# Kernel optimization log

Measured on AMD Instinct MI355X. Metric: run time of the kernel, lower is better.

Reference implementation:

```python
import jax, jax.numpy as jnp
import numpy as np

B, N, C = 1024, 65, 1024
H = 16
D = C // H  # head dim = 64
HIDDEN = 4 * C
EPS = 1e-5


def layer_norm(x, g, b):
    mu = jnp.mean(x, axis=-1, keepdims=True)
    var = jnp.var(x, axis=-1, keepdims=True)
    return (x - mu) * jax.lax.rsqrt(var + EPS) * g + b


def setup_inputs() -> dict:
    key = jax.random.key(0)
    ks = jax.random.split(key, 12)
    s = 0.02
    return {
        "x": jax.random.normal(ks[0], (B, N, C), dtype=jnp.float32),
        "ln1_g": jnp.ones((C,), jnp.float32),
        "ln1_b": jnp.zeros((C,), jnp.float32),
        "qkv_w": jax.random.normal(ks[1], (3 * C, C), jnp.float32) * s,
        "qkv_b": jnp.zeros((3 * C,), jnp.float32),
        "proj_w": jax.random.normal(ks[2], (C, C), jnp.float32) * s,
        "proj_b": jnp.zeros((C,), jnp.float32),
        "attn_bias": jax.random.normal(ks[3], (H, N, N), jnp.float32) * 0.1,
        "bias_scale": jnp.asarray(1.0, jnp.float32),
        "ln2_g": jnp.ones((C,), jnp.float32),
        "ln2_b": jnp.zeros((C,), jnp.float32),
        "fc1_w": jax.random.normal(ks[4], (HIDDEN, C), jnp.float32) * s,
        "fc1_b": jnp.zeros((HIDDEN,), jnp.float32),
        "fc2_w": jax.random.normal(ks[5], (C, HIDDEN), jnp.float32) * s,
        "fc2_b": jnp.zeros((C,), jnp.float32),
    }


def reference(x, ln1_g, ln1_b, qkv_w, qkv_b, proj_w, proj_b, attn_bias,
              bias_scale, ln2_g, ln2_b, fc1_w, fc1_b, fc2_w, fc2_b):
    scale = D ** -0.5
    # --- attention branch: pre-LN ---
    h = layer_norm(x, ln1_g, ln1_b)
    qkv = h @ qkv_w.T + qkv_b                      # [B,N,3C]
    qkv = qkv.reshape(B, N, 3, H, D)
    q = jnp.transpose(qkv[:, :, 0], (0, 2, 1, 3))  # [B,H,N,D]
    k = jnp.transpose(qkv[:, :, 1], (0, 2, 1, 3))
    v = jnp.transpose(qkv[:, :, 2], (0, 2, 1, 3))
    logits = jnp.einsum('bhnd,bhmd->bhnm', q, k) * scale
    logits = logits + bias_scale * attn_bias[None]  # learned per-head 65x65 bias
    attn = jax.nn.softmax(logits, axis=-1)
    o = jnp.einsum('bhnm,bhmd->bhnd', attn, v)      # [B,H,N,D]
    o = jnp.transpose(o, (0, 2, 1, 3)).reshape(B, N, C)
    x = x + (o @ proj_w.T + proj_b)
    # --- MLP branch: pre-LN ---
    h = layer_norm(x, ln2_g, ln2_b)
    h = h @ fc1_w.T + fc1_b
    h = jax.nn.gelu(h, approximate=True)            # tanh GELU, matches F.gelu(approximate='tanh')
    h = h @ fc2_w.T + fc2_b
    return x + h
```

## Files before the change

kernel.cpp:

```cpp
#include <hip/hip_runtime.h>
#include <hip/hip_bf16.h>
#include <cstdint>

typedef __attribute__((ext_vector_type(8))) short bf16x8;
typedef __attribute__((ext_vector_type(8))) unsigned short ushort8;
typedef __attribute__((ext_vector_type(4))) float f32x4;

__device__ __forceinline__ unsigned short f2bf(float f) {
    unsigned u = __builtin_bit_cast(unsigned, f);
    u += 0x7FFFu + ((u >> 16) & 1u);
    return (unsigned short)(u >> 16);
}
__device__ __forceinline__ float bf2f(unsigned short s) {
    unsigned u = ((unsigned)s) << 16;
    return __builtin_bit_cast(float, u);
}

__device__ __forceinline__ void gld16(const unsigned short* g, unsigned short* l) {
    __builtin_amdgcn_global_load_lds(
        (const __attribute__((address_space(1))) void*)g,
        (__attribute__((address_space(3))) void*)l, 16, 0, 0);
}

#define BARRIER    asm volatile("s_barrier" ::: "memory")
#define WAITLGKM0  asm volatile("s_waitcnt lgkmcnt(0)" ::: "memory")
#define WAITVM6    asm volatile("s_waitcnt vmcnt(6)" ::: "memory")

__global__ __launch_bounds__(256) void cvt_w(const float* __restrict__ s,
                                             unsigned short* __restrict__ d, int n4) {
    int i = blockIdx.x * 256 + threadIdx.x;
    if (i >= n4) return;
    float4 v = ((const float4*)s)[i];
    ushort4 o = make_ushort4(f2bf(v.x), f2bf(v.y), f2bf(v.z), f2bf(v.w));
    ((ushort4*)d)[i] = o;
}

__global__ __launch_bounds__(256) void ln_bf16(const float* __restrict__ x,
                                               const float* __restrict__ g,
                                               const float* __restrict__ bta,
                                               unsigned short* __restrict__ out) {
    const int row = blockIdx.x;
    const int t = threadIdx.x;
    const float4 v = ((const float4*)(x + (size_t)row * 1024))[t];
    float s  = v.x + v.y + v.z + v.w;
    float ss = v.x*v.x + v.y*v.y + v.z*v.z + v.w*v.w;
#pragma unroll
    for (int off = 32; off > 0; off >>= 1) {
        s  += __shfl_down(s,  off, 64);
        ss += __shfl_down(ss, off, 64);
    }
    __shared__ float red[8];
    if ((t & 63) == 0) { red[t >> 6] = s; red[4 + (t >> 6)] = ss; }
    __syncthreads();
    const float S  = red[0] + red[1] + red[2] + red[3];
    const float SS = red[4] + red[5] + red[6] + red[7];
    const float mu = S * (1.0f / 1024.0f);
    const float rs = rsqrtf(SS * (1.0f / 1024.0f) - mu * mu + 1e-5f);
    const float4 gv = ((const float4*)g)[t];
    const float4 bv = ((const float4*)bta)[t];
    ushort4 o = make_ushort4(f2bf((v.x - mu) * rs * gv.x + bv.x),
                             f2bf((v.y - mu) * rs * gv.y + bv.y),
                             f2bf((v.z - mu) * rs * gv.z + bv.z),
                             f2bf((v.w - mu) * rs * gv.w + bv.w));
    ((ushort4*)(out + (size_t)row * 1024))[t] = o;
}

template <int MODE>
__global__ __launch_bounds__(512, 2) void gemm8p(const unsigned short* __restrict__ A,
                                                 const unsigned short* __restrict__ W,
                                                 const float* __restrict__ bias,
                                                 const float* __restrict__ res,
                                                 void* __restrict__ outv,
                                                 int N, int K) {
    __shared__ __align__(128) unsigned short lA[4][8192];
    __shared__ __align__(128) unsigned short lB[4][8192];
    const int t = threadIdx.x;
    const int lane = t & 63;
    const int wave = t >> 6;
    const int wm = wave >> 2, wn = wave & 3;

    const int nwg  = gridDim.x * gridDim.y;
    const int orig = blockIdx.y * gridDim.x + blockIdx.x;
    const int id   = (orig & 7) * (nwg >> 3) + (orig >> 3);
    const int bx   = id % gridDim.x;
    const int by   = id / gridDim.x;
    const long row0 = (long)by * 256;
    const long col0 = (long)bx * 256;

    const int srow  = wave * 16 + (lane >> 3);
    const int sslot = (lane & 7) ^ ((lane >> 3) & 7);
    const unsigned short* gA = A + (row0 + srow) * (long)K + sslot * 8;
    const unsigned short* gW = W + (col0 + srow) * (long)K + sslot * 8;
    const int lwo = wave * 1024;

#define STG_A(H, TILE, SLOT) do { \
    const unsigned short* _g = gA + (long)(H) * 128 * K + (long)(TILE) * 64; \
    unsigned short* _l = &lA[(SLOT) * 2 + (H)][lwo]; \
    gld16(_g, _l); gld16(_g + 8L * K, _l + 512); } while (0)
#define STG_B(H, TILE, SLOT) do { \
    const unsigned short* _g = gW + (long)(H) * 128 * K + (long)(TILE) * 64; \
    unsigned short* _l = &lB[(SLOT) * 2 + (H)][lwo]; \
    gld16(_g, _l); gld16(_g + 8L * K, _l + 512); } while (0)

    const int NT = K >> 6;
    const int I  = NT >> 1;

    const int arow = lane & 15;
    const int khi  = lane >> 4;
    const int low7 = lane & 7;

    f32x4 acc[8][4] = {};
    bf16x8 af[4][2], bf0[2][2], bf1[2][2];

    STG_A(0, 0, 0); STG_B(0, 0, 0); STG_B(1, 0, 0); STG_A(1, 0, 0);
    STG_A(0, 1, 1); STG_B(0, 1, 1); STG_B(1, 1, 1);
    WAITVM6;
    BARRIER;

    for (int j = 0; j < I; ++j) {
        const bool stN = (j + 1) < I;
#pragma unroll
        for (int tp = 0; tp < 2; ++tp) {
            const int s2 = tp * 2;
            const int tN = 2 * j + 2 + tp;
            const bool stA1 = (2 * j + tp + 1) < NT;

#pragma unroll
            for (int fi = 0; fi < 4; ++fi) {
                const int r = wm * 64 + fi * 16 + arow;
#pragma unroll
                for (int ks = 0; ks < 2; ++ks)
                    af[fi][ks] = *(const bf16x8*)&lA[s2][r * 64 + (((ks * 4 + khi) ^ low7) << 3)];
            }
#pragma unroll
            for (int fj = 0; fj < 2; ++fj) {
                const int r = wn * 32 + fj * 16 + arow;
#pragma unroll
                for (int ks = 0; ks < 2; ++ks)
                    bf0[fj][ks] = *(const bf16x8*)&lB[s2][r * 64 + (((ks * 4 + khi) ^ low7) << 3)];
            }
            if (stA1) STG_A(1, 2 * j + tp + 1, tp ^ 1);
            BARRIER;
            __builtin_amdgcn_s_setprio(1);
#pragma unroll
            for (int fi = 0; fi < 4; ++fi)
#pragma unroll
                for (int fj = 0; fj < 2; ++fj)
#pragma unroll
                    for (int ks = 0; ks < 2; ++ks)
                        acc[fi][fj] = __builtin_amdgcn_mfma_f32_16x16x32_bf16(af[fi][ks], bf0[fj][ks], acc[fi][fj], 0, 0, 0);
            __builtin_amdgcn_s_setprio(0);
            WAITLGKM0;
            BARRIER;

#pragma unroll
            for (int fj = 0; fj < 2; ++fj) {
                const int r = wn * 32 + fj * 16 + arow;
#pragma unroll
                for (int ks = 0; ks < 2; ++ks)
                    bf1[fj][ks] = *(const bf16x8*)&lB[s2 + 1][r * 64 + (((ks * 4 + khi) ^ low7) << 3)];
            }
            if (stN) STG_A(0, tN, tp);
            BARRIER;
            __builtin_amdgcn_s_setprio(1);
#pragma unroll
            for (int fi = 0; fi < 4; ++fi)
#pragma unroll
                for (int fj = 0; fj < 2; ++fj)
#pragma unroll
                    for (int ks = 0; ks < 2; ++ks)
                        acc[fi][2 + fj] = __builtin_amdgcn_mfma_f32_16x16x32_bf16(af[fi][ks], bf1[fj][ks], acc[fi][2 + fj], 0, 0, 0);
            __builtin_amdgcn_s_setprio(0);
            WAITLGKM0;
            BARRIER;

#pragma unroll
            for (int fi = 0; fi < 4; ++fi) {
                const int r = wm * 64 + fi * 16 + arow;
#pragma unroll
                for (int ks = 0; ks < 2; ++ks)
                    af[fi][ks] = *(const bf16x8*)&lA[s2 + 1][r * 64 + (((ks * 4 + khi) ^ low7) << 3)];
            }
            if (stN) STG_B(0, tN, tp);
            BARRIER;
            __builtin_amdgcn_s_setprio(1);
#pragma unroll
            for (int fi = 0; fi < 4; ++fi)
#pragma unroll
                for (int fj = 0; fj < 2; ++fj)
#pragma unroll
                    for (int ks = 0; ks < 2; ++ks)
                        acc[4 + fi][2 + fj] = __builtin_amdgcn_mfma_f32_16x16x32_bf16(af[fi][ks], bf1[fj][ks], acc[4 + fi][2 + fj], 0, 0, 0);
            __builtin_amdgcn_s_setprio(0);
            WAITLGKM0;
            BARRIER;

            if (stN) STG_B(1, tN, tp);
            BARRIER;
            __builtin_amdgcn_s_setprio(1);
#pragma unroll
            for (int fi = 0; fi < 4; ++fi)
#pragma unroll
                for (int fj = 0; fj < 2; ++fj)
#pragma unroll
                    for (int ks = 0; ks < 2; ++ks)
                        acc[4 + fi][fj] = __builtin_amdgcn_mfma_f32_16x16x32_bf16(af[fi][ks], bf0[fj][ks], acc[4 + fi][fj], 0, 0, 0);
            __builtin_amdgcn_s_setprio(0);
            WAITVM6;
            WAITLGKM0;
            BARRIER;
        }
    }

    const int r4 = khi * 4;
#pragma unroll
    for (int jj = 0; jj < 4; ++jj) {
        const long col = col0 + (jj >> 1) * 128 + wn * 32 + (jj & 1) * 16 + arow;
        const float bj = bias[col];
#pragma unroll
        for (int i = 0; i < 8; ++i) {
            const long rowb = row0 + (i >> 2) * 128 + wm * 64 + (i & 3) * 16 + r4;
#pragma unroll
            for (int r = 0; r < 4; ++r) {
                const long row = rowb + r;
                float val = acc[i][jj][r] + bj;
                if (MODE == 2) {
                    float u = 1.5957691216057308f * (val + 0.044715f * val * val * val);
                    float e = __expf(u);
                    float th = 1.0f - 2.0f / (e + 1.0f);
                    val = 0.5f * val * (1.0f + th);
                }
                if (MODE == 1) {
                    ((float*)outv)[row * N + col] = res[row * N + col] + val;
                } else {
                    ((unsigned short*)outv)[row * N + col] = f2bf(val);
                }
            }
        }
    }
#undef STG_A
#undef STG_B
}

#define SSTR 68
__global__ __launch_bounds__(256) void attn(const unsigned short* __restrict__ qkv,
                                            const float* __restrict__ abias,
                                            const float* __restrict__ bscale_p,
                                            unsigned short* __restrict__ o) {
    const int bh = blockIdx.x;
    const int b = bh >> 4, h = bh & 15;
    const int t = threadIdx.x;
    __shared__ __align__(16) float sq[65 * SSTR];
    __shared__ __align__(16) float sk[65 * SSTR];
    __shared__ __align__(16) unsigned short sv[65 * SSTR];
    __shared__ float ss[65 * 65];
    const size_t base = (size_t)b * 65 * 3072 + h * 64;
    for (int idx = t; idx < 65 * 64; idx += 256) {
        int n = idx >> 6, d = idx & 63;
        size_t g = base + (size_t)n * 3072 + d;
        sq[n * SSTR + d] = bf2f(qkv[g]);
        sk[n * SSTR + d] = bf2f(qkv[g + 1024]);
        sv[n * SSTR + d] = qkv[g + 2048];
    }
    __syncthreads();
    const float bs = bscale_p[0];
    const float* bias_h = abias + h * 65 * 65;
    for (int p = t; p < 65 * 65; p += 256) {
        int i = p % 65, j = p / 65;
        const float4* q4 = (const float4*)&sq[i * SSTR];
        const float4* k4 = (const float4*)&sk[j * SSTR];
        float ax = 0.f, ay = 0.f, az = 0.f, aw = 0.f;
#pragma unroll
        for (int c = 0; c < 16; c++) {
            float4 a = q4[c], bb = k4[c];
            ax += a.x * bb.x; ay += a.y * bb.y; az += a.z * bb.z; aw += a.w * bb.w;
        }
        ss[i * 65 + j] = (ax + ay + az + aw) * 0.125f + bs * bias_h[i * 65 + j];
    }
    __syncthreads();
    if (t < 65) {
        float* r = &ss[t * 65];
        float m = -1e30f;
        for (int j = 0; j < 65; j++) m = fmaxf(m, r[j]);
        float sum = 0.f;
        for (int j = 0; j < 65; j++) { float e = __expf(r[j] - m); r[j] = e; sum += e; }
        float inv = 1.0f / sum;
        for (int j = 0; j < 65; j++) r[j] *= inv;
    }
    __syncthreads();
    for (int p = t; p < 65 * 16; p += 256) {
        int i = p % 65, d4 = p / 65;
        float ax = 0.f, ay = 0.f, az = 0.f, aw = 0.f;
        for (int j = 0; j < 65; j++) {
            float pv = ss[i * 65 + j];
            ushort4 vv = *(const ushort4*)&sv[j * SSTR + d4 * 4];
            ax += pv * bf2f(vv.x); ay += pv * bf2f(vv.y);
            az += pv * bf2f(vv.z); aw += pv * bf2f(vv.w);
        }
        size_t go = (size_t)(b * 65 + i) * 1024 + h * 64 + d4 * 4;
        *(ushort4*)&o[go] = make_ushort4(f2bf(ax), f2bf(ay), f2bf(az), f2bf(aw));
    }
}

extern "C" void kernel_launch(void* const* d_in, const int* in_sizes, int n_in,
                              void* d_out, int out_size, void* d_ws, size_t ws_size,
                              hipStream_t stream) {
    const float* x      = (const float*)d_in[0];
    const float* ln1_g  = (const float*)d_in[1];
    const float* ln1_b  = (const float*)d_in[2];
    const float* qkv_w  = (const float*)d_in[3];
    const float* qkv_b  = (const float*)d_in[4];
    const float* proj_w = (const float*)d_in[5];
    const float* proj_b = (const float*)d_in[6];
    const float* abias  = (const float*)d_in[7];
    const float* bscale = (const float*)d_in[8];
    const float* ln2_g  = (const float*)d_in[9];
    const float* ln2_b  = (const float*)d_in[10];
    const float* fc1_w  = (const float*)d_in[11];
    const float* fc1_b  = (const float*)d_in[12];
    const float* fc2_w  = (const float*)d_in[13];
    const float* fc2_b  = (const float*)d_in[14];
    float* out = (float*)d_out;

    char* ws = (char*)d_ws;
    unsigned short* qkvbuf = (unsigned short*)(ws);
    unsigned short* hbuf   = (unsigned short*)(ws + 545259520ULL);
    unsigned short* wqkv   = (unsigned short*)(ws + 681574400ULL);
    unsigned short* wproj  = (unsigned short*)(ws + 687865856ULL);
    unsigned short* wfc1   = (unsigned short*)(ws + 689963008ULL);
    unsigned short* wfc2   = (unsigned short*)(ws + 698351616ULL);

    const int M = 66560;

    cvt_w<<<3072, 256, 0, stream>>>(qkv_w,  wqkv,  786432);
    cvt_w<<<1024, 256, 0, stream>>>(proj_w, wproj, 262144);
    cvt_w<<<4096, 256, 0, stream>>>(fc1_w,  wfc1,  1048576);
    cvt_w<<<4096, 256, 0, stream>>>(fc2_w,  wfc2,  1048576);

    ln_bf16<<<M, 256, 0, stream>>>(x, ln1_g, ln1_b, hbuf);
    gemm8p<0><<<dim3(12, 260), 512, 0, stream>>>(hbuf, wqkv, qkv_b, nullptr,
                                                 (void*)qkvbuf, 3072, 1024);
    attn<<<16384, 256, 0, stream>>>(qkvbuf, abias, bscale, hbuf);
    gemm8p<1><<<dim3(4, 260), 512, 0, stream>>>(hbuf, wproj, proj_b, x,
                                                (void*)out, 1024, 1024);
    ln_bf16<<<M, 256, 0, stream>>>(out, ln2_g, ln2_b, hbuf);
    gemm8p<2><<<dim3(16, 260), 512, 0, stream>>>(hbuf, wfc1, fc1_b, nullptr,
                                                 (void*)qkvbuf, 4096, 1024);
    gemm8p<1><<<dim3(4, 260), 512, 0, stream>>>(qkvbuf, wfc2, fc2_b, out,
                                                (void*)out, 1024, 4096);
}
```

Before: 3.720 ms.

## Rewrite attention kernel with MFMA tiles for QK^T and PV

Replaces the scalar fp32 attention kernel with one that computes QK^T and P·V using 16x16x32 bf16 MFMA instructions on 16-row tiles padded to 80 rows and 96 columns. Q and K are staged in LDS as bf16 with 16-byte loads, and V is stored transposed with zero padding. Softmax is spread over four lanes per row with shuffle reductions, writes unnormalised bf16 probabilities, and applies the 1/sum scale at output. The change is meant to cut the per-head dot-product cost and LDS traffic. In exchange, probabilities are rounded to bf16 before P·V, and the kernel uses more LDS with aliased buffers.

```diff
diff --git a/kernel.cpp b/kernel.cpp
--- a/kernel.cpp
+++ b/kernel.cpp
@@ -242,63 +242,117 @@
 #undef STG_B
 }
 
-#define SSTR 68
-__global__ __launch_bounds__(256) void attn(const unsigned short* __restrict__ qkv,
-                                            const float* __restrict__ abias,
-                                            const float* __restrict__ bscale_p,
-                                            unsigned short* __restrict__ o) {
+__global__ __launch_bounds__(256, 3) void attn_mfma(const unsigned short* __restrict__ qkv,
+                                                    const float* __restrict__ abias,
+                                                    const float* __restrict__ bscale_p,
+                                                    unsigned short* __restrict__ o) {
     const int bh = blockIdx.x;
     const int b = bh >> 4, h = bh & 15;
     const int t = threadIdx.x;
-    __shared__ __align__(16) float sq[65 * SSTR];
-    __shared__ __align__(16) float sk[65 * SSTR];
-    __shared__ __align__(16) unsigned short sv[65 * SSTR];
-    __shared__ float ss[65 * 65];
+    const int lane = t & 63;
+    const int wave = t >> 6;
+
+    __shared__ __align__(16) char smem[53252];
+    unsigned short* lq = (unsigned short*)smem;
+    unsigned short* lk = (unsigned short*)(smem + 11520);
+    float* ss          = (float*)smem;
+    unsigned short* vt = (unsigned short*)(smem + 23040);
+    unsigned short* lp = (unsigned short*)(smem + 36352);
+    float* sinv        = (float*)(smem + 52992);
+
     const size_t base = (size_t)b * 65 * 3072 + h * 64;
-    for (int idx = t; idx < 65 * 64; idx += 256) {
-        int n = idx >> 6, d = idx & 63;
-        size_t g = base + (size_t)n * 3072 + d;
-        sq[n * SSTR + d] = bf2f(qkv[g]);
-        sk[n * SSTR + d] = bf2f(qkv[g + 1024]);
-        sv[n * SSTR + d] = qkv[g + 2048];
-    }
+    for (int c = t; c < 520; c += 256) {
+        const int row = c >> 3, s = c & 7;
+        const size_t g = base + (size_t)row * 3072 + s * 8;
+        *(ushort8*)&lq[row * 72 + s * 8] = *(const ushort8*)&qkv[g];
+        *(ushort8*)&lk[row * 72 + s * 8] = *(const ushort8*)&qkv[g + 1024];
+        ushort8 vv = *(const ushort8*)&qkv[g + 2048];
+#pragma unroll
+        for (int e = 0; e < 8; e++) vt[(s * 8 + e) * 104 + row] = vv[e];
+    }
+    for (int c = t; c < 2048; c += 256) vt[(c >> 5) * 104 + 65 + (c & 31)] = 0;
+    for (int c = t; c < 2080; c += 256) lp[(c >> 5) * 104 + 65 + (c & 31)] = 0;
     __syncthreads();
+
+    const int arow = lane & 15;
+    const int khi8 = (lane >> 4) * 8;
+    const int r4   = (lane >> 4) * 4;
+
+    f32x4 acc[7];
+#pragma unroll
+    for (int c = 0; c < 7; c++) {
+        const int tt = wave + 4 * c;
+        if (tt < 25) {
+            const int ti = tt / 5, tj = tt % 5;
+            f32x4 a = {};
+#pragma unroll
+            for (int ks = 0; ks < 2; ks++) {
+                bf16x8 af = *(const bf16x8*)&lq[(ti * 16 + arow) * 72 + khi8 + ks * 32];
+                bf16x8 bf = *(const bf16x8*)&lk[(tj * 16 + arow) * 72 + khi8 + ks * 32];
+                a = __builtin_amdgcn_mfma_f32_16x16x32_bf16(af, bf, a, 0, 0, 0);
+            }
+            acc[c] = a;
+        }
+    }
+    __syncthreads();
+
     const float bs = bscale_p[0];
     const float* bias_h = abias + h * 65 * 65;
-    for (int p = t; p < 65 * 65; p += 256) {
-        int i = p % 65, j = p / 65;
-        const float4* q4 = (const float4*)&sq[i * SSTR];
-        const float4* k4 = (const float4*)&sk[j * SSTR];
-        float ax = 0.f, ay = 0.f, az = 0.f, aw = 0.f;
-#pragma unroll
-        for (int c = 0; c < 16; c++) {
-            float4 a = q4[c], bb = k4[c];
-            ax += a.x * bb.x; ay += a.y * bb.y; az += a.z * bb.z; aw += a.w * bb.w;
-        }
-        ss[i * 65 + j] = (ax + ay + az + aw) * 0.125f + bs * bias_h[i * 65 + j];
+#pragma unroll
+    for (int c = 0; c < 7; c++) {
+        const int tt = wave + 4 * c;
+        if (tt < 25) {
+            const int ti = tt / 5, tj = tt % 5;
+            const int j = tj * 16 + arow;
+            const int bj = j < 65 ? j : 64;
+#pragma unroll
+            for (int r = 0; r < 4; r++) {
+                const int i = ti * 16 + r4 + r;
+                const int bi = i < 65 ? i : 64;
+                const float val = acc[c][r] * 0.125f + bs * bias_h[bi * 65 + bj];
+                if (i < 65) ss[i * 84 + j] = val;
+            }
+        }
     }
     __syncthreads();
-    if (t < 65) {
-        float* r = &ss[t * 65];
-        float m = -1e30f;
-        for (int j = 0; j < 65; j++) m = fmaxf(m, r[j]);
-        float sum = 0.f;
-        for (int j = 0; j < 65; j++) { float e = __expf(r[j] - m); r[j] = e; sum += e; }
-        float inv = 1.0f / sum;
-        for (int j = 0; j < 65; j++) r[j] *= inv;
+
+    {
+        const int l4 = t & 3;
+        for (int r = t >> 2; r < 65; r += 64) {
+            float m = -1e30f;
+            for (int j = l4; j < 65; j += 4) m = fmaxf(m, ss[r * 84 + j]);
+            m = fmaxf(m, __shfl_xor(m, 1, 64));
+            m = fmaxf(m, __shfl_xor(m, 2, 64));
+            float sum = 0.f;
+            for (int j = l4; j < 65; j += 4) {
+                const float e = __expf(ss[r * 84 + j] - m);
+                lp[r * 104 + j] = f2bf(e);
+                sum += e;
+            }
+            sum += __shfl_xor(sum, 1, 64);
+            sum += __shfl_xor(sum, 2, 64);
+            if (l4 == 0) sinv[r] = 1.0f / sum;
+        }
     }
     __syncthreads();
-    for (int p = t; p < 65 * 16; p += 256) {
-        int i = p % 65, d4 = p / 65;
-        float ax = 0.f, ay = 0.f, az = 0.f, aw = 0.f;
-        for (int j = 0; j < 65; j++) {
-            float pv = ss[i * 65 + j];
-            ushort4 vv = *(const ushort4*)&sv[j * SSTR + d4 * 4];
-            ax += pv * bf2f(vv.x); ay += pv * bf2f(vv.y);
-            az += pv * bf2f(vv.z); aw += pv * bf2f(vv.w);
-        }
-        size_t go = (size_t)(b * 65 + i) * 1024 + h * 64 + d4 * 4;
-        *(ushort4*)&o[go] = make_ushort4(f2bf(ax), f2bf(ay), f2bf(az), f2bf(aw));
+
+#pragma unroll
+    for (int c = 0; c < 5; c++) {
+        const int ti = c, tj = wave;
+        f32x4 a = {};
+#pragma unroll
+        for (int ks = 0; ks < 3; ks++) {
+            bf16x8 pf = *(const bf16x8*)&lp[(ti * 16 + arow) * 104 + khi8 + ks * 32];
+            bf16x8 vf = *(const bf16x8*)&vt[(tj * 16 + arow) * 104 + khi8 + ks * 32];
+            a = __builtin_amdgcn_mfma_f32_16x16x32_bf16(pf, vf, a, 0, 0, 0);
+        }
+        const int d = tj * 16 + arow;
+#pragma unroll
+        for (int r = 0; r < 4; r++) {
+            const int i = ti * 16 + r4 + r;
+            if (i < 65)
+                o[((size_t)(b * 65 + i)) * 1024 + h * 64 + d] = f2bf(a[r] * sinv[i]);
+        }
     }
 }
 
@@ -340,7 +394,7 @@
     ln_bf16<<<M, 256, 0, stream>>>(x, ln1_g, ln1_b, hbuf);
     gemm8p<0><<<dim3(12, 260), 512, 0, stream>>>(hbuf, wqkv, qkv_b, nullptr,
                                                  (void*)qkvbuf, 3072, 1024);
-    attn<<<16384, 256, 0, stream>>>(qkvbuf, abias, bscale, hbuf);
+    attn_mfma<<<16384, 256, 0, stream>>>(qkvbuf, abias, bscale, hbuf);
     gemm8p<1><<<dim3(4, 260), 512, 0, stream>>>(hbuf, wproj, proj_b, x,
                                                 (void*)out, 1024, 1024);
     ln_bf16<<<M, 256, 0, stream>>>(out, ln2_g, ln2_b, hbuf);
```

After: 3.078 ms. 17.3% less time.
